# Performance work log

Hardware: AMD Instinct MI355X
Metric: run time of the kernel (lower is better)

The kernel has to match this reference:

```python
import jax, jax.numpy as jnp
import numpy as np

T, B, D_IN, D_H, D_OUT = 16, 8192, 512, 1024, 256


def setup_inputs() -> dict:
    key = jax.random.key(0)
    ks = jax.random.split(key, 4)
    # He-style scaled init to keep activations sane
    x = jax.random.normal(ks[0], (B, D_IN), dtype=jnp.float32)
    W1 = jax.random.normal(ks[1], (T, D_IN, D_H), dtype=jnp.float32) / np.sqrt(D_IN)
    b1 = jnp.zeros((T, D_H), dtype=jnp.float32)
    W2 = jax.random.normal(ks[2], (T, D_H, D_H), dtype=jnp.float32) / np.sqrt(D_H)
    b2 = jnp.zeros((T, D_H), dtype=jnp.float32)
    W3 = jax.random.normal(ks[3], (T, D_H, D_OUT), dtype=jnp.float32) / np.sqrt(D_H)
    b3 = jnp.zeros((T, D_OUT), dtype=jnp.float32)
    return {"x": x, "W1": W1, "b1": b1, "W2": W2, "b2": b2, "W3": W3, "b3": b3}


def reference(x, W1, b1, W2, b2, W3, b3):
    # Batched over the tree dimension t: one grouped GEMM per layer instead of
    # a Python loop over trees.
    h = jax.nn.relu(jnp.einsum('bi,tih->tbh', x, W1) + b1[:, None, :])   # [T,B,H]
    h = jax.nn.relu(jnp.einsum('tbh,thk->tbk', h, W2) + b2[:, None, :])  # [T,B,H]
    out = jnp.einsum('tbh,tho->tbo', h, W3) + b3[:, None, :]             # [T,B,O]
    return jnp.mean(out, axis=0)                                          # [B,O]
```

## Files before the change

kernel.cpp:

```cpp
#include <hip/hip_runtime.h>
#include <hip/hip_bf16.h>
#include <stdint.h>

#define T_TREES 16
#define B_ROWS  8192
#define DIN     512
#define DH      1024
#define DOUT    256

typedef unsigned short u16;
typedef __attribute__((ext_vector_type(8))) short short8;
typedef __attribute__((ext_vector_type(16))) float floatx16;

__device__ __forceinline__ u16 f2bf(float f) {
    union { float f; uint32_t u; } v; v.f = f;
    uint32_t u = v.u;
    uint32_t r = (u + 0x7fffu + ((u >> 16) & 1u)) >> 16;
    return (u16)r;
}

__device__ __forceinline__ void async_copy16(const u16* g, u16* l) {
    __builtin_amdgcn_global_load_lds(
        (const __attribute__((address_space(1))) uint32_t*)g,
        (__attribute__((address_space(3))) uint32_t*)l,
        16, 0, 0);
}

__global__ void prep_kernel(const float* __restrict__ x, u16* __restrict__ xb,
                            const float* __restrict__ b3, float* __restrict__ out,
                            const float* __restrict__ W1, const float* __restrict__ W2,
                            const float* __restrict__ W3,
                            u16* __restrict__ W1b, u16* __restrict__ W2b,
                            u16* __restrict__ W3b) {
    __shared__ float tile[32][33];
    if (blockIdx.x < 4096) {
        int idx = blockIdx.x * 256 + threadIdx.x;
        float4 v = ((const float4*)x)[idx];
        ushort4 o;
        o.x = f2bf(v.x); o.y = f2bf(v.y); o.z = f2bf(v.z); o.w = f2bf(v.w);
        ((ushort4*)xb)[idx] = o;
    } else if (blockIdx.x < 12288) {
        int idx = (blockIdx.x - 4096) * 256 + threadIdx.x;
        int o = idx & (DOUT - 1);
        float s = 0.f;
#pragma unroll
        for (int t = 0; t < T_TREES; t++) s += b3[t * DOUT + o];
        out[idx] = s * (1.f / T_TREES);
    } else {
        int bid = blockIdx.x - 12288;
        int t = bid / 1792, tl = bid - t * 1792;
        const float* in; u16* outp; int K, N, kt, nt; float scale = 1.f;
        if (tl < 512)       { in = W1; outp = W1b; K = DIN; N = DH;   kt = tl & 15; nt = tl >> 4; }
        else if (tl < 1536) { tl -= 512;  in = W2; outp = W2b; K = DH; N = DH;   kt = tl & 31; nt = tl >> 5; }
        else                { tl -= 1536; in = W3; outp = W3b; K = DH; N = DOUT; kt = tl & 31; nt = tl >> 5;
                              scale = 1.f / T_TREES; }
        int k0 = kt * 32, n0 = nt * 32;
        const float* inb = in + (size_t)t * K * N;
        u16* outb = outp + (size_t)t * K * N;
        int c = threadIdx.x & 31, rg = threadIdx.x >> 5;
#pragma unroll
        for (int i = 0; i < 4; i++) {
            int r = rg * 4 + i;
            tile[r][c] = inb[(size_t)(k0 + r) * N + n0 + c];
        }
        __syncthreads();
#pragma unroll
        for (int i = 0; i < 4; i++) {
            int r = rg * 4 + i;
            outb[(size_t)(n0 + r) * K + k0 + c] = f2bf(tile[c][r] * scale);
        }
    }
}

__global__ void reduce_kernel(const float* __restrict__ Part, float* __restrict__ Out, int g) {
    int idx = blockIdx.x * 256 + threadIdx.x;
    float4 s = ((const float4*)Out)[idx];
    for (int t = 0; t < g; t++) {
        float4 p = ((const float4*)(Part + (size_t)t * B_ROWS * DOUT))[idx];
        s.x += p.x; s.y += p.y; s.z += p.z; s.w += p.w;
    }
    ((float4*)Out)[idx] = s;
}


#define GEMM_PREAMBLE()                                          \
    const int tid = threadIdx.x;                                 \
    const int wave = tid >> 6;                                   \
    const int lane = tid & 63;                                   \
    const int l31 = lane & 31;                                   \
    const int h = lane >> 5;                                     \
    const int rb = l31 & 3;                                      \
    const int wm = (wave >> 1) * 64;                             \
    const int wn = (wave & 1) * 64;                              \
    const int s = lane >> 3;                                     \
    const int c8 = lane & 7;                                     \
    const int colElem = ((c8 ^ ((s & 3) << 1)) << 3);

#define GEMM_KSLAB(Ab, Bb, K)                                                         \
    {                                                                                  \
        _Pragma("unroll")                                                              \
        for (int i = 0; i < 4; i++) {                                                  \
            const int j = wave * 4 + i;                                                \
            const int r = j * 8 + s;                                                   \
            async_copy16(Ab + (size_t)(m0 + r) * K + kk + colElem, &ldsA[j * 512]);    \
            async_copy16(Bb + (size_t)(n0 + r) * K + kk + colElem, &ldsB[j * 512]);    \
        }                                                                              \
        __syncthreads();                                                               \
        _Pragma("unroll")                                                              \
        for (int kq = 0; kq < 4; kq++) {                                               \
            const int col = ((kq ^ rb) << 4) + h * 8;                                  \
            short8 a[2], b[2];                                                         \
            _Pragma("unroll")                                                          \
            for (int fi = 0; fi < 2; fi++)                                             \
                a[fi] = *(const short8*)&ldsA[(wm + fi * 32 + l31) * 64 + col];        \
            _Pragma("unroll")                                                          \
            for (int fj = 0; fj < 2; fj++)                                             \
                b[fj] = *(const short8*)&ldsB[(wn + fj * 32 + l31) * 64 + col];        \
            _Pragma("unroll")                                                          \
            for (int fi = 0; fi < 2; fi++)                                             \
                _Pragma("unroll")                                                      \
                for (int fj = 0; fj < 2; fj++)                                         \
                    acc[fi][fj] = __builtin_amdgcn_mfma_f32_32x32x16_bf16(             \
                        a[fi], b[fj], acc[fi][fj], 0, 0, 0);                           \
        }                                                                              \
        __syncthreads();                                                               \
    }

__global__ __launch_bounds__(256, 2)
void gemm_relu_bf16(const u16* __restrict__ A, size_t aStrideT,
                    const u16* __restrict__ Bt,
                    const float* __restrict__ bias,
                    u16* __restrict__ C,
                    int M, int N, int K) {
    __shared__ u16 ldsA[128 * 64];
    __shared__ u16 ldsB[128 * 64];

    const int t = blockIdx.z;
    const u16* Ab = A + (size_t)t * aStrideT;
    const u16* Bb = Bt + (size_t)t * (size_t)N * K;
    u16* Cb = C + (size_t)t * (size_t)M * N;
    const float* biasb = bias + (size_t)t * N;

    const int m0 = blockIdx.x * 128;
    const int n0 = blockIdx.y * 128;

    GEMM_PREAMBLE();

    floatx16 acc[2][2];
#pragma unroll
    for (int fi = 0; fi < 2; fi++)
#pragma unroll
        for (int fj = 0; fj < 2; fj++)
#pragma unroll
            for (int r = 0; r < 16; r++) acc[fi][fj][r] = 0.f;

    for (int kk = 0; kk < K; kk += 64) GEMM_KSLAB(Ab, Bb, K);

#pragma unroll
    for (int fj = 0; fj < 2; fj++) {
        const int n = n0 + wn + fj * 32 + l31;
        const float bv = biasb[n];
#pragma unroll
        for (int fi = 0; fi < 2; fi++) {
#pragma unroll
            for (int r = 0; r < 16; r++) {
                const int m = m0 + wm + fi * 32 + (r & 3) + 8 * (r >> 2) + 4 * h;
                float v = acc[fi][fj][r] + bv;
                v = v > 0.f ? v : 0.f;
                Cb[(size_t)m * N + n] = f2bf(v);
            }
        }
    }
}

__global__ __launch_bounds__(256, 2)
void gemm_final_part(const u16* __restrict__ H2, const u16* __restrict__ W3t,
                     float* __restrict__ Part) {
    constexpr int M = B_ROWS, N = DOUT, K = DH;
    __shared__ u16 ldsA[128 * 64];
    __shared__ u16 ldsB[128 * 64];

    const int m0 = blockIdx.x * 128;
    const int n0 = blockIdx.y * 128;
    const int t = blockIdx.z;
    const u16* Ab = H2 + (size_t)t * M * K;
    const u16* Bb = W3t + (size_t)t * N * K;
    float* Pb = Part + (size_t)t * M * N;

    GEMM_PREAMBLE();

    floatx16 acc[2][2];
#pragma unroll
    for (int fi = 0; fi < 2; fi++)
#pragma unroll
        for (int fj = 0; fj < 2; fj++)
#pragma unroll
            for (int r = 0; r < 16; r++) acc[fi][fj][r] = 0.f;

    for (int kk = 0; kk < K; kk += 64) GEMM_KSLAB(Ab, Bb, K);

#pragma unroll
    for (int fj = 0; fj < 2; fj++) {
        const int n = n0 + wn + fj * 32 + l31;
#pragma unroll
        for (int fi = 0; fi < 2; fi++) {
#pragma unroll
            for (int r = 0; r < 16; r++) {
                const int m = m0 + wm + fi * 32 + (r & 3) + 8 * (r >> 2) + 4 * h;
                Pb[(size_t)m * N + n] = acc[fi][fj][r];
            }
        }
    }
}

extern "C" void kernel_launch(void* const* d_in, const int* in_sizes, int n_in,
                              void* d_out, int out_size, void* d_ws, size_t ws_size,
                              hipStream_t stream) {
    const float* x  = (const float*)d_in[0];
    const float* W1 = (const float*)d_in[1];
    const float* b1 = (const float*)d_in[2];
    const float* W2 = (const float*)d_in[3];
    const float* b2 = (const float*)d_in[4];
    const float* W3 = (const float*)d_in[5];
    const float* b3 = (const float*)d_in[6];
    float* out = (float*)d_out;

    const size_t XB_BYTES = 8388608ull;
    const size_t W1B_BYTES = 16777216ull, W2B_BYTES = 33554432ull, W3B_BYTES = 8388608ull;
    const size_t FIXED = XB_BYTES + W1B_BYTES + W2B_BYTES + W3B_BYTES;
    const size_t PER_TREE = 33554432ull;

    uint8_t* ws = (uint8_t*)d_ws;
    u16* xb  = (u16*)ws;
    u16* W1b = (u16*)(ws + XB_BYTES);
    u16* W2b = (u16*)(ws + XB_BYTES + W1B_BYTES);
    u16* W3b = (u16*)(ws + XB_BYTES + W1B_BYTES + W2B_BYTES);
    u16* h1  = (u16*)(ws + FIXED);
    float* part = (float*)(ws + FIXED);

    int g = 16;
    while (g > 1 && FIXED + (size_t)g * PER_TREE > ws_size) g >>= 1;
    const int nG = T_TREES / g;
    u16* h2 = (u16*)(ws + FIXED + (size_t)g * (PER_TREE / 2));

    prep_kernel<<<12288 + 1792 * T_TREES, 256, 0, stream>>>(
        x, xb, b3, out, W1, W2, W3, W1b, W2b, W3b);

    for (int gi = 0; gi < nG; gi++) {
        const int t0 = gi * g;
        gemm_relu_bf16<<<dim3(B_ROWS / 128, DH / 128, g), 256, 0, stream>>>(
            xb, 0, W1b + (size_t)t0 * DIN * DH, b1 + (size_t)t0 * DH, h1, B_ROWS, DH, DIN);
        gemm_relu_bf16<<<dim3(B_ROWS / 128, DH / 128, g), 256, 0, stream>>>(
            h1, (size_t)B_ROWS * DH, W2b + (size_t)t0 * DH * DH, b2 + (size_t)t0 * DH, h2, B_ROWS, DH, DH);
        gemm_final_part<<<dim3(B_ROWS / 128, DOUT / 128, g), 256, 0, stream>>>(
            h2, W3b + (size_t)t0 * DH * DOUT, part);
        reduce_kernel<<<(B_ROWS * DOUT / 4) / 256, 256, 0, stream>>>(part, out, g);
    }
}
```

Baseline: 817.9 us.

## Use 256x256 tiles with double-buffered async LDS pipeline in GEMMs

Replaces the 128x128, 256-thread GEMM tiles with 256x256 tiles computed by 512 threads (8 waves, 2x4 layout). K-slabs are loaded into a double-buffered 128KB dynamic LDS region via async global-to-LDS copies, with vmcnt-based waits, so the next slab's loads overlap the current slab's MFMAs. The change also adds a new XOR swizzle and s_setprio around the MFMA bursts. The goal is more operand reuse per byte loaded and less load/barrier stall. The cost is much higher LDS and register use per block, which limits occupancy to about one block per CU. The layer-3 grid also shrinks to a single N tile.

```diff
diff --git a/kernel.cpp b/kernel.cpp
--- a/kernel.cpp
+++ b/kernel.cpp
@@ -83,57 +83,85 @@
 }
 
 
-#define GEMM_PREAMBLE()                                          \
-    const int tid = threadIdx.x;                                 \
-    const int wave = tid >> 6;                                   \
-    const int lane = tid & 63;                                   \
-    const int l31 = lane & 31;                                   \
-    const int h = lane >> 5;                                     \
-    const int rb = l31 & 3;                                      \
-    const int wm = (wave >> 1) * 64;                             \
-    const int wn = (wave & 1) * 64;                              \
-    const int s = lane >> 3;                                     \
-    const int c8 = lane & 7;                                     \
-    const int colElem = ((c8 ^ ((s & 3) << 1)) << 3);
-
-#define GEMM_KSLAB(Ab, Bb, K)                                                         \
+#define GEMM256_PREAMBLE()                                   \
+    const int tid  = threadIdx.x;                            \
+    const int wave = tid >> 6;                               \
+    const int lane = tid & 63;                               \
+    const int l31  = lane & 31;                              \
+    const int h    = lane >> 5;                              \
+    const int wm2  = wave >> 2;                              \
+    const int wn4  = wave & 3;                               \
+    const int rg   = tid >> 3;                               \
+    const int colE = (((tid & 7) ^ (rg & 7)) << 3);          \
+    const int xm   = l31 & 7;
+
+#define STAGE(kt_, p_)                                                                 \
     {                                                                                  \
+        const int k0_ = (kt_) * 64;                                                    \
+        u16* lA_ = lds + (p_) * 32768 + wave * 512;                                    \
+        u16* lB_ = lA_ + 16384;                                                        \
         _Pragma("unroll")                                                              \
-        for (int i = 0; i < 4; i++) {                                                  \
-            const int j = wave * 4 + i;                                                \
-            const int r = j * 8 + s;                                                   \
-            async_copy16(Ab + (size_t)(m0 + r) * K + kk + colElem, &ldsA[j * 512]);    \
-            async_copy16(Bb + (size_t)(n0 + r) * K + kk + colElem, &ldsB[j * 512]);    \
+        for (int j_ = 0; j_ < 4; j_++) {                                               \
+            const int row_ = j_ * 64 + rg;                                             \
+            async_copy16(Ab + (size_t)(m0 + row_) * K + k0_ + colE, lA_ + j_ * 4096);  \
+            async_copy16(Bb + (size_t)(n0 + row_) * K + k0_ + colE, lB_ + j_ * 4096);  \
         }                                                                              \
-        __syncthreads();                                                               \
+    }
+
+#define COMPUTE(p_)                                                                    \
+    {                                                                                  \
+        const u16* A_ = lds + (p_) * 32768;                                            \
+        const u16* B_ = A_ + 16384;                                                    \
+        short8 bfr[2][4];                                                              \
         _Pragma("unroll")                                                              \
-        for (int kq = 0; kq < 4; kq++) {                                               \
-            const int col = ((kq ^ rb) << 4) + h * 8;                                  \
-            short8 a[2], b[2];                                                         \
+        for (int nf = 0; nf < 2; nf++) {                                               \
+            const int r_ = wn4 * 64 + nf * 32 + l31;                                   \
             _Pragma("unroll")                                                          \
-            for (int fi = 0; fi < 2; fi++)                                             \
-                a[fi] = *(const short8*)&ldsA[(wm + fi * 32 + l31) * 64 + col];        \
+            for (int kk = 0; kk < 4; kk++)                                             \
+                bfr[nf][kk] = *(const short8*)&B_[r_ * 64 + (((kk * 2 + h) ^ xm) << 3)]; \
+        }                                                                              \
+        _Pragma("unroll")                                                              \
+        for (int mh = 0; mh < 2; mh++) {                                               \
+            short8 afr[2][4];                                                          \
             _Pragma("unroll")                                                          \
-            for (int fj = 0; fj < 2; fj++)                                             \
-                b[fj] = *(const short8*)&ldsB[(wn + fj * 32 + l31) * 64 + col];        \
+            for (int mf = 0; mf < 2; mf++) {                                           \
+                const int r_ = wm2 * 128 + mh * 64 + mf * 32 + l31;                    \
+                _Pragma("unroll")                                                      \
+                for (int kk = 0; kk < 4; kk++)                                         \
+                    afr[mf][kk] = *(const short8*)&A_[r_ * 64 + (((kk * 2 + h) ^ xm) << 3)]; \
+            }                                                                          \
+            __builtin_amdgcn_s_setprio(1);                                             \
             _Pragma("unroll")                                                          \
-            for (int fi = 0; fi < 2; fi++)                                             \
+            for (int kk = 0; kk < 4; kk++)                                             \
                 _Pragma("unroll")                                                      \
-                for (int fj = 0; fj < 2; fj++)                                         \
-                    acc[fi][fj] = __builtin_amdgcn_mfma_f32_32x32x16_bf16(             \
-                        a[fi], b[fj], acc[fi][fj], 0, 0, 0);                           \
+                for (int mf = 0; mf < 2; mf++)                                         \
+                    _Pragma("unroll")                                                  \
+                    for (int nf = 0; nf < 2; nf++)                                     \
+                        acc[mh * 2 + mf][nf] = __builtin_amdgcn_mfma_f32_32x32x16_bf16(\
+                            afr[mf][kk], bfr[nf][kk], acc[mh * 2 + mf][nf], 0, 0, 0);  \
+            __builtin_amdgcn_s_setprio(0);                                             \
         }                                                                              \
-        __syncthreads();                                                               \
-    }
-
-__global__ __launch_bounds__(256, 2)
+    }
+
+#define GEMM256_MAIN()                                                           \
+    STAGE(0, 0);                                                                 \
+    STAGE(1, 1);                                                                 \
+    for (int kt = 0; kt < NT; kt++) {                                            \
+        const int p_ = kt & 1;                                                   \
+        if (kt < NT - 1) asm volatile("s_waitcnt vmcnt(8)\n\ts_barrier" ::: "memory"); \
+        else             asm volatile("s_waitcnt vmcnt(0)\n\ts_barrier" ::: "memory"); \
+        COMPUTE(p_);                                                             \
+        asm volatile("s_barrier" ::: "memory");                                  \
+        if (kt + 2 < NT) STAGE(kt + 2, p_);                                      \
+    }
+
+__global__ __launch_bounds__(512, 2)
 void gemm_relu_bf16(const u16* __restrict__ A, size_t aStrideT,
                     const u16* __restrict__ Bt,
                     const float* __restrict__ bias,
                     u16* __restrict__ C,
                     int M, int N, int K) {
-    __shared__ u16 ldsA[128 * 64];
-    __shared__ u16 ldsB[128 * 64];
+    extern __shared__ u16 lds[];
 
     const int t = blockIdx.z;
     const u16* Ab = A + (size_t)t * aStrideT;
@@ -141,31 +169,32 @@
     u16* Cb = C + (size_t)t * (size_t)M * N;
     const float* biasb = bias + (size_t)t * N;
 
-    const int m0 = blockIdx.x * 128;
-    const int n0 = blockIdx.y * 128;
-
-    GEMM_PREAMBLE();
-
-    floatx16 acc[2][2];
-#pragma unroll
-    for (int fi = 0; fi < 2; fi++)
-#pragma unroll
-        for (int fj = 0; fj < 2; fj++)
-#pragma unroll
-            for (int r = 0; r < 16; r++) acc[fi][fj][r] = 0.f;
-
-    for (int kk = 0; kk < K; kk += 64) GEMM_KSLAB(Ab, Bb, K);
-
-#pragma unroll
-    for (int fj = 0; fj < 2; fj++) {
-        const int n = n0 + wn + fj * 32 + l31;
+    const int m0 = blockIdx.x * 256;
+    const int n0 = blockIdx.y * 256;
+
+    GEMM256_PREAMBLE();
+
+    floatx16 acc[4][2];
+#pragma unroll
+    for (int ai = 0; ai < 4; ai++)
+#pragma unroll
+        for (int nf = 0; nf < 2; nf++)
+#pragma unroll
+            for (int r = 0; r < 16; r++) acc[ai][nf][r] = 0.f;
+
+    const int NT = K >> 6;
+    GEMM256_MAIN();
+
+#pragma unroll
+    for (int nf = 0; nf < 2; nf++) {
+        const int n = n0 + wn4 * 64 + nf * 32 + l31;
         const float bv = biasb[n];
 #pragma unroll
-        for (int fi = 0; fi < 2; fi++) {
+        for (int ai = 0; ai < 4; ai++) {
 #pragma unroll
             for (int r = 0; r < 16; r++) {
-                const int m = m0 + wm + fi * 32 + (r & 3) + 8 * (r >> 2) + 4 * h;
-                float v = acc[fi][fj][r] + bv;
+                const int m = m0 + wm2 * 128 + ai * 32 + (r & 3) + 8 * (r >> 2) + 4 * h;
+                float v = acc[ai][nf][r] + bv;
                 v = v > 0.f ? v : 0.f;
                 Cb[(size_t)m * N + n] = f2bf(v);
             }
@@ -173,41 +202,41 @@
     }
 }
 
-__global__ __launch_bounds__(256, 2)
+__global__ __launch_bounds__(512, 2)
 void gemm_final_part(const u16* __restrict__ H2, const u16* __restrict__ W3t,
                      float* __restrict__ Part) {
     constexpr int M = B_ROWS, N = DOUT, K = DH;
-    __shared__ u16 ldsA[128 * 64];
-    __shared__ u16 ldsB[128 * 64];
-
-    const int m0 = blockIdx.x * 128;
-    const int n0 = blockIdx.y * 128;
+    extern __shared__ u16 lds[];
+
+    const int m0 = blockIdx.x * 256;
+    const int n0 = blockIdx.y * 256;
     const int t = blockIdx.z;
     const u16* Ab = H2 + (size_t)t * M * K;
     const u16* Bb = W3t + (size_t)t * N * K;
     float* Pb = Part + (size_t)t * M * N;
 
-    GEMM_PREAMBLE();
-
-    floatx16 acc[2][2];
-#pragma unroll
-    for (int fi = 0; fi < 2; fi++)
-#pragma unroll
-        for (int fj = 0; fj < 2; fj++)
-#pragma unroll
-            for (int r = 0; r < 16; r++) acc[fi][fj][r] = 0.f;
-
-    for (int kk = 0; kk < K; kk += 64) GEMM_KSLAB(Ab, Bb, K);
-
-#pragma unroll
-    for (int fj = 0; fj < 2; fj++) {
-        const int n = n0 + wn + fj * 32 + l31;
-#pragma unroll
-        for (int fi = 0; fi < 2; fi++) {
+    GEMM256_PREAMBLE();
+
+    floatx16 acc[4][2];
+#pragma unroll
+    for (int ai = 0; ai < 4; ai++)
+#pragma unroll
+        for (int nf = 0; nf < 2; nf++)
+#pragma unroll
+            for (int r = 0; r < 16; r++) acc[ai][nf][r] = 0.f;
+
+    const int NT = K >> 6;
+    GEMM256_MAIN();
+
+#pragma unroll
+    for (int nf = 0; nf < 2; nf++) {
+        const int n = n0 + wn4 * 64 + nf * 32 + l31;
+#pragma unroll
+        for (int ai = 0; ai < 4; ai++) {
 #pragma unroll
             for (int r = 0; r < 16; r++) {
-                const int m = m0 + wm + fi * 32 + (r & 3) + 8 * (r >> 2) + 4 * h;
-                Pb[(size_t)m * N + n] = acc[fi][fj][r];
+                const int m = m0 + wm2 * 128 + ai * 32 + (r & 3) + 8 * (r >> 2) + 4 * h;
+                Pb[(size_t)m * N + n] = acc[ai][nf][r];
             }
         }
     }
@@ -246,13 +275,15 @@
     prep_kernel<<<12288 + 1792 * T_TREES, 256, 0, stream>>>(
         x, xb, b3, out, W1, W2, W3, W1b, W2b, W3b);
 
+    const uint32_t LDS_BYTES = 131072;
+
     for (int gi = 0; gi < nG; gi++) {
         const int t0 = gi * g;
-        gemm_relu_bf16<<<dim3(B_ROWS / 128, DH / 128, g), 256, 0, stream>>>(
+        gemm_relu_bf16<<<dim3(B_ROWS / 256, DH / 256, g), 512, LDS_BYTES, stream>>>(
             xb, 0, W1b + (size_t)t0 * DIN * DH, b1 + (size_t)t0 * DH, h1, B_ROWS, DH, DIN);
-        gemm_relu_bf16<<<dim3(B_ROWS / 128, DH / 128, g), 256, 0, stream>>>(
+        gemm_relu_bf16<<<dim3(B_ROWS / 256, DH / 256, g), 512, LDS_BYTES, stream>>>(
             h1, (size_t)B_ROWS * DH, W2b + (size_t)t0 * DH * DH, b2 + (size_t)t0 * DH, h2, B_ROWS, DH, DH);
-        gemm_final_part<<<dim3(B_ROWS / 128, DOUT / 128, g), 256, 0, stream>>>(
+        gemm_final_part<<<dim3(B_ROWS / 256, DOUT / 256, g), 512, LDS_BYTES, stream>>>(
             h2, W3b + (size_t)t0 * DH * DOUT, part);
         reduce_kernel<<<(B_ROWS * DOUT / 4) / 256, 256, 0, stream>>>(part, out, g);
     }
```

Measured after the change: 849.4 us. 1.04x slower.
